# Optimization experiments

Measured on AMD Instinct MI355X. Metric: run time of the kernel, lower is better.

## Reference

```python
import jax, jax.numpy as jnp
import numpy as np

N, T, D, H = 4, 2048, 1024, 16
DK = D // H

def setup_inputs() -> dict:
    key = jax.random.key(0)
    k1, k2, k3 = jax.random.split(key, 3)
    z = jax.random.normal(k1, (N, T, D), dtype=jnp.float32)
    Wqkv = jax.random.normal(k2, (D, 3 * D), dtype=jnp.float32) * 0.01
    Wout = jax.random.normal(k3, (D, D), dtype=jnp.float32) * 0.01
    return {"z": z, "Wqkv": Wqkv, "Wout": Wout}

def reference(z, Wqkv, Wout):
    n, t, d = z.shape
    scale = DK ** -0.5
    qkv = z @ Wqkv  # [N,T,3D]
    q, k, v = jnp.split(qkv, 3, axis=-1)
    # [N,T,D] -> [N,H,T,dk]
    q = q.reshape(n, t, H, DK).transpose(0, 2, 1, 3)
    k = k.reshape(n, t, H, DK).transpose(0, 2, 1, 3)
    v = v.reshape(n, t, H, DK).transpose(0, 2, 1, 3)
    attn = jnp.einsum('nhqd,nhkd->nhqk', q, k) * scale
    causal = jnp.tril(jnp.ones((t, t), dtype=bool))
    attn = jnp.where(causal, attn, -jnp.inf)
    attn = jax.nn.softmax(attn, axis=-1)
    out = jnp.einsum('nhqk,nhkd->nhqd', attn, v)  # [N,H,T,dk]
    out = out.transpose(0, 2, 1, 3).reshape(n, t, d)
    return out @ Wout
```

## Files before the change

kernel.cpp:

```cpp
#include <hip/hip_runtime.h>
#include <hip/hip_bf16.h>

typedef __bf16 bf16;
typedef __bf16 bf16x8 __attribute__((ext_vector_type(8)));
typedef float f32x4 __attribute__((ext_vector_type(4)));

#define N_B 4
#define T_S 2048
#define D_M 1024
#define H_N 16
#define D_K 64
#define D3 3072
#define NEG_BIG (-1e30f)
#define QSCALE 0.18033688011112042f

#if __has_builtin(__builtin_amdgcn_exp2f)
#define EXP2(x) __builtin_amdgcn_exp2f(x)
#else
#define EXP2(x) exp2f(x)
#endif

__device__ __forceinline__ void gload_lds16(const bf16* g, bf16* l) {
    __builtin_amdgcn_global_load_lds((const __attribute__((address_space(1))) void*)g,
                                     (__attribute__((address_space(3))) void*)l, 16, 0, 0);
}

__device__ __forceinline__ bool probe_fp32(const void* p) {
    const unsigned int* w = (const unsigned int*)p;
    int weird = 0;
#pragma unroll
    for (int i = 0; i < 16; ++i) {
        unsigned int v = w[i];
        unsigned int e = (v >> 7) & 0xFFu;
        if ((v & 0xFFFFu) != 0u && (e < 100u || e > 140u)) weird++;
    }
    return weird >= 4;
}

__global__ __launch_bounds__(256) void prep(const void* __restrict__ z, bf16* __restrict__ zb,
                                            const void* __restrict__ Wqkv, bf16* __restrict__ WqkvT,
                                            const void* __restrict__ Wout, bf16* __restrict__ WoutT) {
    __shared__ bf16 tile[32][33];
    const int b = blockIdx.x;
    const int t = threadIdx.x;

    if (b < 4096) {
        const int i = (b * 256 + t) * 8;
        if (probe_fp32(z)) {
            const float* zf = (const float*)z;
            float4 u0 = *(const float4*)(zf + i);
            float4 u1 = *(const float4*)(zf + i + 4);
            union { uint4 q; bf16 h[8]; } pk;
            pk.h[0] = (bf16)u0.x; pk.h[1] = (bf16)u0.y;
            pk.h[2] = (bf16)u0.z; pk.h[3] = (bf16)u0.w;
            pk.h[4] = (bf16)u1.x; pk.h[5] = (bf16)u1.y;
            pk.h[6] = (bf16)u1.z; pk.h[7] = (bf16)u1.w;
            *(uint4*)(zb + i) = pk.q;
        } else {
            *(uint4*)(zb + i) = ((const uint4*)z)[b * 256 + t];
        }
        return;
    }

    const void* in; bf16* out; int R, C, c0, r0;
    if (b < 7168) {
        int idx = b - 4096;
        in = Wqkv; out = WqkvT; R = 1024; C = 3072;
        c0 = (idx % 96) * 32; r0 = (idx / 96) * 32;
    } else {
        int idx = b - 7168;
        in = Wout; out = WoutT; R = 1024; C = 1024;
        c0 = (idx & 31) * 32; r0 = (idx >> 5) * 32;
    }
    const int tx = t & 31, ty = t >> 5;
    if (probe_fp32(in)) {
        const float* inf_ = (const float*)in;
        for (int i = 0; i < 4; ++i)
            tile[ty + i * 8][tx] = (bf16)inf_[(size_t)(r0 + ty + i * 8) * C + c0 + tx];
    } else {
        const bf16* inb = (const bf16*)in;
        for (int i = 0; i < 4; ++i)
            tile[ty + i * 8][tx] = inb[(size_t)(r0 + ty + i * 8) * C + c0 + tx];
    }
    __syncthreads();
    for (int i = 0; i < 4; ++i)
        out[(size_t)(c0 + ty + i * 8) * R + r0 + tx] = tile[tx][ty + i * 8];
}

__global__ __launch_bounds__(512, 2) void gemm256(const bf16* __restrict__ A,
                                                  const bf16* __restrict__ Bt,
                                                  void* __restrict__ C,
                                                  bf16* __restrict__ Kf,
                                                  bf16* __restrict__ Vf,
                                                  int M, int N, int K,
                                                  int modeC) {
    __shared__ bf16 As[3][256 * 64];
    __shared__ bf16 Bs[3][128 * 64];
    const int t = threadIdx.x;
    const int m0 = blockIdx.y * 256, n0 = blockIdx.x * 128;
    const int w = t >> 6, lane = t & 63, quad = lane >> 4, l15 = lane & 15;
    const int wr = (w >> 1) * 64, wc = (w & 1) * 64;
    const int sr = t >> 3;
    const int sg = ((t & 7) ^ (sr & 7)) * 8;
    const int xorL = (l15 & 7) * 8;

    const bf16* a0 = A + (size_t)(m0 + sr) * K + sg;
    const bf16* a1 = A + (size_t)(m0 + 64 + sr) * K + sg;
    const bf16* a2 = A + (size_t)(m0 + 128 + sr) * K + sg;
    const bf16* a3 = A + (size_t)(m0 + 192 + sr) * K + sg;
    const bf16* b0 = Bt + (size_t)(n0 + sr) * K + sg;
    const bf16* b1 = Bt + (size_t)(n0 + 64 + sr) * K + sg;
    const int ldsOff = w * 512;

    f32x4 acc[4][4];
    const f32x4 zero4 = {0.f, 0.f, 0.f, 0.f};
#pragma unroll
    for (int i = 0; i < 4; ++i)
#pragma unroll
        for (int j = 0; j < 4; ++j) acc[i][j] = zero4;

    const int nt = K >> 6;

    gload_lds16(a0, &As[0][0 * 4096 + ldsOff]);
    gload_lds16(a1, &As[0][1 * 4096 + ldsOff]);
    gload_lds16(a2, &As[0][2 * 4096 + ldsOff]);
    gload_lds16(a3, &As[0][3 * 4096 + ldsOff]);
    gload_lds16(b0, &Bs[0][0 * 4096 + ldsOff]);
    gload_lds16(b1, &Bs[0][1 * 4096 + ldsOff]);
    if (nt > 1) {
        gload_lds16(a0 + 64, &As[1][0 * 4096 + ldsOff]);
        gload_lds16(a1 + 64, &As[1][1 * 4096 + ldsOff]);
        gload_lds16(a2 + 64, &As[1][2 * 4096 + ldsOff]);
        gload_lds16(a3 + 64, &As[1][3 * 4096 + ldsOff]);
        gload_lds16(b0 + 64, &Bs[1][0 * 4096 + ldsOff]);
        gload_lds16(b1 + 64, &Bs[1][1 * 4096 + ldsOff]);
        asm volatile("s_waitcnt vmcnt(6)" ::: "memory");
    } else {
        asm volatile("s_waitcnt vmcnt(0)" ::: "memory");
    }
    __builtin_amdgcn_sched_barrier(0);
    __builtin_amdgcn_s_barrier();
    __builtin_amdgcn_sched_barrier(0);

    int cur = 0;
    for (int tt = 0; tt < nt; ++tt) {
        const bf16* Ac = As[cur];
        const bf16* Bc = Bs[cur];
        int pf = cur + 2; if (pf >= 3) pf -= 3;
        const bool do_pf = (tt + 2 < nt);
        const int kpf = (tt + 2) << 6;

        {
            const int colOff = (quad * 8) ^ xorL;
            bf16x8 af[4], bfv[4];
#pragma unroll
            for (int i = 0; i < 4; ++i)
                af[i] = *(const bf16x8*)(Ac + (wr + i * 16 + l15) * 64 + colOff);
#pragma unroll
            for (int j = 0; j < 4; ++j)
                bfv[j] = *(const bf16x8*)(Bc + (wc + j * 16 + l15) * 64 + colOff);
            if (do_pf) {
                gload_lds16(a0 + kpf, &As[pf][0 * 4096 + ldsOff]);
                gload_lds16(a1 + kpf, &As[pf][1 * 4096 + ldsOff]);
                gload_lds16(a2 + kpf, &As[pf][2 * 4096 + ldsOff]);
            }
            __builtin_amdgcn_sched_barrier(0);
            __builtin_amdgcn_s_barrier();
            asm volatile("s_waitcnt lgkmcnt(0)" ::: "memory");
            __builtin_amdgcn_sched_barrier(0);
            __builtin_amdgcn_s_setprio(1);
#pragma unroll
            for (int i = 0; i < 4; ++i)
#pragma unroll
                for (int j = 0; j < 4; ++j)
                    acc[i][j] = __builtin_amdgcn_mfma_f32_16x16x32_bf16(af[i], bfv[j], acc[i][j], 0, 0, 0);
            __builtin_amdgcn_s_setprio(0);
            __builtin_amdgcn_sched_barrier(0);
            __builtin_amdgcn_s_barrier();
            __builtin_amdgcn_sched_barrier(0);
        }

        {
            const int colOff = (32 + quad * 8) ^ xorL;
            bf16x8 af[4], bfv[4];
#pragma unroll
            for (int i = 0; i < 4; ++i)
                af[i] = *(const bf16x8*)(Ac + (wr + i * 16 + l15) * 64 + colOff);
#pragma unroll
            for (int j = 0; j < 4; ++j)
                bfv[j] = *(const bf16x8*)(Bc + (wc + j * 16 + l15) * 64 + colOff);
            if (do_pf) {
                gload_lds16(a3 + kpf, &As[pf][3 * 4096 + ldsOff]);
                gload_lds16(b0 + kpf, &Bs[pf][0 * 4096 + ldsOff]);
                gload_lds16(b1 + kpf, &Bs[pf][1 * 4096 + ldsOff]);
                asm volatile("s_waitcnt vmcnt(6)" ::: "memory");
            } else {
                asm volatile("s_waitcnt vmcnt(0)" ::: "memory");
            }
            __builtin_amdgcn_sched_barrier(0);
            __builtin_amdgcn_s_barrier();
            asm volatile("s_waitcnt lgkmcnt(0)" ::: "memory");
            __builtin_amdgcn_sched_barrier(0);
            __builtin_amdgcn_s_setprio(1);
#pragma unroll
            for (int i = 0; i < 4; ++i)
#pragma unroll
                for (int j = 0; j < 4; ++j)
                    acc[i][j] = __builtin_amdgcn_mfma_f32_16x16x32_bf16(af[i], bfv[j], acc[i][j], 0, 0, 0);
            __builtin_amdgcn_s_setprio(0);
            __builtin_amdgcn_sched_barrier(0);
            __builtin_amdgcn_s_barrier();
            __builtin_amdgcn_sched_barrier(0);
        }
        cur = cur + 1; if (cur == 3) cur = 0;
    }

    if (modeC == 1) {
        float* Cf = (float*)C;
        for (int i = 0; i < 4; ++i)
            for (int fc = 0; fc < 4; ++fc)
                for (int r = 0; r < 4; ++r)
                    Cf[(size_t)(m0 + wr + i * 16 + quad * 4 + r) * N
                       + (n0 + wc + fc * 16 + l15)] = acc[i][fc][r];
    } else if (n0 < 1024) {
        bf16* q = (bf16*)C;
        for (int i = 0; i < 4; ++i)
            for (int fc = 0; fc < 4; ++fc)
                for (int r = 0; r < 4; ++r)
                    q[(size_t)(m0 + wr + i * 16 + quad * 4 + r) * 1024
                      + (n0 + wc + fc * 16 + l15)] = (bf16)(acc[i][fc][r] * QSCALE);
    } else if (n0 < 2048) {
        for (int i = 0; i < 4; ++i) {
            int rowb = m0 + wr + i * 16 + quad * 4;
            int nb = rowb >> 11, tt = rowb & 2047;
            int kt = tt >> 6, f = (tt >> 4) & 3, l15k = tt & 15;
            for (int fc = 0; fc < 4; ++fc) {
                int col = n0 + wc + fc * 16 + l15 - 1024;
                int h = col >> 6, dk = col & 63;
                int ks = dk >> 5, qdk = (dk >> 3) & 3, j = dk & 7;
                size_t base = ((size_t)((nb * 16 + h) * 32 + kt) * 8 + ks * 4 + f) * 512 + j;
                for (int r = 0; r < 4; ++r)
                    Kf[base + (qdk * 16 + l15k + r) * 8] = (bf16)acc[i][fc][r];
            }
        }
    } else {
        for (int i = 0; i < 4; ++i) {
            int rowb = m0 + wr + i * 16 + quad * 4;
            int nb = rowb >> 11, tt = rowb & 2047;
            int kt = tt >> 6, ks = (tt >> 5) & 1, qdv = (tt >> 3) & 3, j0 = tt & 7;
            for (int fc = 0; fc < 4; ++fc) {
                int col = n0 + wc + fc * 16 + l15 - 2048;
                int h = col >> 6, dl = col & 63;
                int fv = dl >> 4, l15v = dl & 15;
                union { ushort4 u; bf16 hh[4]; } pk;
                for (int r = 0; r < 4; ++r) pk.hh[r] = (bf16)acc[i][fc][r];
                *(ushort4*)(Vf + ((size_t)((nb * 16 + h) * 32 + kt) * 8 + ks * 4 + fv) * 512
                            + (qdv * 16 + l15v) * 8 + j0) = pk.u;
            }
        }
    }
}

#define LDP 72
__global__ __launch_bounds__(256, 2) void attn_fused(const bf16* __restrict__ q,
                                                     const bf16* __restrict__ Kf,
                                                     const bf16* __restrict__ Vf,
                                                     bf16* __restrict__ attn_out) {
    __shared__ bf16 Ks[2][4096];
    __shared__ bf16 Vs[2][4096];
    __shared__ bf16 Pl[4 * 32 * LDP];

    const int b = blockIdx.x;
    const int head = b & 63;
    const int qt = 15 - (b >> 6);
    const int n = head >> 4, h = head & 15;
    const int t = threadIdx.x;
    const int w = t >> 6, lane = t & 63, qd = lane >> 4, l15 = lane & 15;
    const int q0w = qt * 128 + w * 32;
    const size_t rowBase = (size_t)n * T_S;
    const bf16* KfH = Kf + (size_t)head * 32 * 4096;
    const bf16* VfH = Vf + (size_t)head * 32 * 4096;
    bf16* Plw = Pl + w * 32 * LDP;
    const int sc = w * 2;

    bf16x8 bQ[2][2];
#pragma unroll
    for (int qh = 0; qh < 2; ++qh)
#pragma unroll
        for (int ks = 0; ks < 2; ++ks)
            bQ[qh][ks] = *(const bf16x8*)(q + (rowBase + q0w + qh * 16 + l15) * 1024
                                          + h * 64 + ks * 32 + qd * 8);

    float l_lane[2] = {0.f, 0.f};
    f32x4 oacc[2][4];
    const f32x4 zero4 = {0.f, 0.f, 0.f, 0.f};
#pragma unroll
    for (int qh = 0; qh < 2; ++qh)
#pragma unroll
        for (int fd = 0; fd < 4; ++fd) oacc[qh][fd] = zero4;

    const int ktmax_w = (q0w + 31) >> 6;
    const int ktmax_b = (qt * 128 + 127) >> 6;

    gload_lds16(KfH + (sc + 0) * 512 + lane * 8, &Ks[0][(sc + 0) * 512]);
    gload_lds16(KfH + (sc + 1) * 512 + lane * 8, &Ks[0][(sc + 1) * 512]);
    gload_lds16(VfH + (sc + 0) * 512 + lane * 8, &Vs[0][(sc + 0) * 512]);
    gload_lds16(VfH + (sc + 1) * 512 + lane * 8, &Vs[0][(sc + 1) * 512]);
    __syncthreads();

    int cur = 0;
    for (int kt = 0; kt <= ktmax_b; ++kt) {
        if (kt + 1 <= ktmax_b) {
            const bf16* Kn = KfH + (size_t)(kt + 1) * 4096;
            const bf16* Vn = VfH + (size_t)(kt + 1) * 4096;
            gload_lds16(Kn + (sc + 0) * 512 + lane * 8, &Ks[cur ^ 1][(sc + 0) * 512]);
            gload_lds16(Kn + (sc + 1) * 512 + lane * 8, &Ks[cur ^ 1][(sc + 1) * 512]);
            gload_lds16(Vn + (sc + 0) * 512 + lane * 8, &Vs[cur ^ 1][(sc + 0) * 512]);
            gload_lds16(Vn + (sc + 1) * 512 + lane * 8, &Vs[cur ^ 1][(sc + 1) * 512]);
        }

        if (kt <= ktmax_w) {
            const int k0r = kt * 64;

            bf16x8 aK[2][4];
#pragma unroll
            for (int fr = 0; fr < 8; ++fr)
                aK[fr >> 2][fr & 3] = *(const bf16x8*)(&Ks[cur][fr * 512 + lane * 8]);

            f32x4 sacc[2][4];
#pragma unroll
            for (int qh = 0; qh < 2; ++qh)
#pragma unroll
                for (int fc = 0; fc < 4; ++fc) sacc[qh][fc] = zero4;
#pragma unroll
            for (int ks = 0; ks < 2; ++ks)
#pragma unroll
                for (int fc = 0; fc < 4; ++fc) {
                    sacc[0][fc] = __builtin_amdgcn_mfma_f32_16x16x32_bf16(aK[ks][fc], bQ[0][ks], sacc[0][fc], 0, 0, 0);
                    sacc[1][fc] = __builtin_amdgcn_mfma_f32_16x16x32_bf16(aK[ks][fc], bQ[1][ks], sacc[1][fc], 0, 0, 0);
                }

            if (k0r + 63 > q0w) {
#pragma unroll
                for (int qh = 0; qh < 2; ++qh) {
                    const int qq = q0w + qh * 16 + l15;
#pragma unroll
                    for (int fc = 0; fc < 4; ++fc)
#pragma unroll
                        for (int rr = 0; rr < 4; ++rr)
                            if (k0r + fc * 16 + qd * 4 + rr > qq) sacc[qh][fc][rr] = NEG_BIG;
                }
            }

#pragma unroll
            for (int qh = 0; qh < 2; ++qh) {
                float rs = 0.f;
#pragma unroll
                for (int fc = 0; fc < 4; ++fc) {
                    union { ushort4 u; bf16 hh[4]; } pk;
#pragma unroll
                    for (int rr = 0; rr < 4; ++rr) {
                        float p = EXP2(sacc[qh][fc][rr]);
                        rs += p;
                        pk.hh[rr] = (bf16)p;
                    }
                    *(ushort4*)(Plw + (qh * 16 + l15) * LDP + fc * 16 + qd * 4) = pk.u;
                }
                l_lane[qh] += rs;
            }

            bf16x8 aV[2][4];
#pragma unroll
            for (int fr = 0; fr < 8; ++fr)
                aV[fr >> 2][fr & 3] = *(const bf16x8*)(&Vs[cur][fr * 512 + lane * 8]);
#pragma unroll
            for (int ks = 0; ks < 2; ++ks) {
                bf16x8 bP0 = *(const bf16x8*)(Plw + l15 * LDP + ks * 32 + qd * 8);
                bf16x8 bP1 = *(const bf16x8*)(Plw + (16 + l15) * LDP + ks * 32 + qd * 8);
#pragma unroll
                for (int fd = 0; fd < 4; ++fd) {
                    oacc[0][fd] = __builtin_amdgcn_mfma_f32_16x16x32_bf16(aV[ks][fd], bP0, oacc[0][fd], 0, 0, 0);
                    oacc[1][fd] = __builtin_amdgcn_mfma_f32_16x16x32_bf16(aV[ks][fd], bP1, oacc[1][fd], 0, 0, 0);
                }
            }
        }

        __syncthreads();
        cur ^= 1;
    }

#pragma unroll
    for (int qh = 0; qh < 2; ++qh) {
        float l = l_lane[qh];
        l += __shfl_xor(l, 16, 64);
        l += __shfl_xor(l, 32, 64);
        float inv = 1.f / l;
#pragma unroll
        for (int fd = 0; fd < 4; ++fd) {
            union { ushort4 u; bf16 hh[4]; } pk;
#pragma unroll
            for (int rr = 0; rr < 4; ++rr) pk.hh[rr] = (bf16)(oacc[qh][fd][rr] * inv);
            *(ushort4*)(attn_out + (rowBase + q0w + qh * 16 + l15) * D_M
                        + h * D_K + fd * 16 + qd * 4) = pk.u;
        }
    }
}

extern "C" void kernel_launch(void* const* d_in, const int* in_sizes, int n_in,
                              void* d_out, int out_size, void* d_ws, size_t ws_size,
                              hipStream_t stream) {
    const void* z    = d_in[0];
    const void* Wqkv = d_in[1];
    const void* Wout = d_in[2];

    char* ws = (char*)d_ws;
    bf16* q     = (bf16*)(ws + 256);
    bf16* attn  = (bf16*)(ws + 256 + 16777216);
    bf16* zb    = attn;
    bf16* WqkvT = (bf16*)(ws + 256 + 2 * 16777216);
    bf16* WoutT = (bf16*)(ws + 256 + 2 * 16777216 + 6291456);

    bf16* Kf = (bf16*)d_out;
    bf16* Vf = Kf + 8388608;

    prep<<<dim3(8192), 256, 0, stream>>>(z, zb, Wqkv, WqkvT, Wout, WoutT);

    gemm256<<<dim3(D3 / 128, (N_B * T_S) / 256), 512, 0, stream>>>(
        zb, WqkvT, q, Kf, Vf, N_B * T_S, D3, D_M, 2);

    attn_fused<<<dim3(64 * 16), 256, 0, stream>>>(q, Kf, Vf, attn);

    gemm256<<<dim3(D_M / 128, (N_B * T_S) / 256), 512, 0, stream>>>(
        attn, WoutT, d_out, Kf, Vf, N_B * T_S, D_M, D_M, 1);
}
```

Before: 225.9 us.

## Triple-buffer K/V tiles in attention with prefetch distance two

The attention kernel's K/V shared-memory staging goes from double to triple buffering, prefetching tile kt+2 while computing tile kt. The full __syncthreads is replaced with explicit vmcnt waits that keep the newest prefetch in flight, plus a raw s_barrier. The aim is to hide global-to-LDS load latency further. It costs 16KB more LDS per block, which may reduce occupancy below the two blocks per CU requested by the launch bounds, and relies on manual waitcnt correctness.

```diff
diff --git a/kernel.cpp b/kernel.cpp
--- a/kernel.cpp
+++ b/kernel.cpp
@@ -266,8 +266,8 @@
                                                      const bf16* __restrict__ Kf,
                                                      const bf16* __restrict__ Vf,
                                                      bf16* __restrict__ attn_out) {
-    __shared__ bf16 Ks[2][4096];
-    __shared__ bf16 Vs[2][4096];
+    __shared__ bf16 Ks[3][4096];
+    __shared__ bf16 Vs[3][4096];
     __shared__ bf16 Pl[4 * 32 * LDP];
 
     const int b = blockIdx.x;
@@ -306,17 +306,31 @@
     gload_lds16(KfH + (sc + 1) * 512 + lane * 8, &Ks[0][(sc + 1) * 512]);
     gload_lds16(VfH + (sc + 0) * 512 + lane * 8, &Vs[0][(sc + 0) * 512]);
     gload_lds16(VfH + (sc + 1) * 512 + lane * 8, &Vs[0][(sc + 1) * 512]);
-    __syncthreads();
+    if (ktmax_b >= 1) {
+        const bf16* K1 = KfH + 4096;
+        const bf16* V1 = VfH + 4096;
+        gload_lds16(K1 + (sc + 0) * 512 + lane * 8, &Ks[1][(sc + 0) * 512]);
+        gload_lds16(K1 + (sc + 1) * 512 + lane * 8, &Ks[1][(sc + 1) * 512]);
+        gload_lds16(V1 + (sc + 0) * 512 + lane * 8, &Vs[1][(sc + 0) * 512]);
+        gload_lds16(V1 + (sc + 1) * 512 + lane * 8, &Vs[1][(sc + 1) * 512]);
+        asm volatile("s_waitcnt vmcnt(4)" ::: "memory");
+    } else {
+        asm volatile("s_waitcnt vmcnt(0)" ::: "memory");
+    }
+    __builtin_amdgcn_sched_barrier(0);
+    __builtin_amdgcn_s_barrier();
+    __builtin_amdgcn_sched_barrier(0);
 
     int cur = 0;
     for (int kt = 0; kt <= ktmax_b; ++kt) {
-        if (kt + 1 <= ktmax_b) {
-            const bf16* Kn = KfH + (size_t)(kt + 1) * 4096;
-            const bf16* Vn = VfH + (size_t)(kt + 1) * 4096;
-            gload_lds16(Kn + (sc + 0) * 512 + lane * 8, &Ks[cur ^ 1][(sc + 0) * 512]);
-            gload_lds16(Kn + (sc + 1) * 512 + lane * 8, &Ks[cur ^ 1][(sc + 1) * 512]);
-            gload_lds16(Vn + (sc + 0) * 512 + lane * 8, &Vs[cur ^ 1][(sc + 0) * 512]);
-            gload_lds16(Vn + (sc + 1) * 512 + lane * 8, &Vs[cur ^ 1][(sc + 1) * 512]);
+        if (kt + 2 <= ktmax_b) {
+            int pf = cur + 2; if (pf >= 3) pf -= 3;
+            const bf16* Kn = KfH + (size_t)(kt + 2) * 4096;
+            const bf16* Vn = VfH + (size_t)(kt + 2) * 4096;
+            gload_lds16(Kn + (sc + 0) * 512 + lane * 8, &Ks[pf][(sc + 0) * 512]);
+            gload_lds16(Kn + (sc + 1) * 512 + lane * 8, &Ks[pf][(sc + 1) * 512]);
+            gload_lds16(Vn + (sc + 0) * 512 + lane * 8, &Vs[pf][(sc + 0) * 512]);
+            gload_lds16(Vn + (sc + 1) * 512 + lane * 8, &Vs[pf][(sc + 1) * 512]);
         }
 
         if (kt <= ktmax_w) {
@@ -385,8 +399,17 @@
             }
         }
 
-        __syncthreads();
-        cur ^= 1;
+        if (kt < ktmax_b) {
+            if (kt + 2 <= ktmax_b) {
+                asm volatile("s_waitcnt vmcnt(4)" ::: "memory");
+            } else {
+                asm volatile("s_waitcnt vmcnt(0)" ::: "memory");
+            }
+            __builtin_amdgcn_sched_barrier(0);
+            __builtin_amdgcn_s_barrier();
+            __builtin_amdgcn_sched_barrier(0);
+        }
+        cur = cur + 1; if (cur == 3) cur = 0;
     }
 
 #pragma unroll
```

Result: slower. 233.0 us (+3.1%).
